# Kernel tuning notes

Measured on AMD Instinct MI355X. Metric: run time of the kernel, lower is better.

## Reference

```python
import jax, jax.numpy as jnp
import numpy as np

N_NODES = 50000
N_EDGES = 800000
D_FEAT = 64


def setup_inputs() -> dict:
    key = jax.random.key(0)
    k_x, k_e, k_w = jax.random.split(key, 3)
    x = jax.random.normal(k_x, (N_NODES, D_FEAT), dtype=jnp.float32)
    edge_index = jax.random.randint(k_e, (2, N_EDGES), 0, N_NODES, dtype=jnp.int64)
    # message MLP params (phi_Theta): single linear + ReLU
    W = jax.random.normal(k_w, (D_FEAT, D_FEAT), dtype=jnp.float32) / np.sqrt(D_FEAT)
    b = jnp.zeros((D_FEAT,), dtype=jnp.float32)
    return {"x": x, "edge_index": edge_index, "W": W, "b": b}


def reference(x, edge_index, W, b):
    # flow = source_to_target: messages flow from edge_index[0] (j) to edge_index[1] (i)
    src = edge_index[0]  # j: source nodes (gather)
    dst = edge_index[1]  # i: target nodes (scatter index)
    n_nodes = x.shape[0]
    # __collect__: index_select gather of source node features -> x_j [E, D]
    x_j = x[src]
    # message: per-edge MLP  phi(x_j) = relu(x_j W + b)
    msg = jax.nn.relu(jnp.einsum('ed,df->ef', x_j, W) + b)
    # aggregate: scatter-add into target nodes (aggr='add', dim_size = size_i)
    out = jax.ops.segment_sum(msg, dst, num_segments=n_nodes)
    # update: identity
    return out
```

## Files before the change

### kernel.cpp

```cpp
#include <hip/hip_runtime.h>
#include <hip/hip_bf16.h>

#define D 64
#define CAP 32
#define OVF_CAP 16384
#define NSHARD 8

__device__ __forceinline__ float bf2f(unsigned short u) {
    return __uint_as_float((unsigned int)u << 16);
}
__device__ __forceinline__ unsigned short f2bf(float f) {
    unsigned int u = __float_as_uint(f);
    unsigned int r = (u + 0x7fffu + ((u >> 16) & 1u)) >> 16;
    return (unsigned short)r;
}

__global__ __launch_bounds__(256) void node_mlp_kernel(
    const float* __restrict__ x, const float* __restrict__ W,
    const float* __restrict__ b, unsigned short* __restrict__ m0,
    unsigned short* __restrict__ m1, int* __restrict__ cnt,
    int* __restrict__ ovf_cnt, int n_nodes) {
    for (int i = blockIdx.x * blockDim.x + threadIdx.x; i < n_nodes;
         i += gridDim.x * blockDim.x) cnt[i] = 0;
    if (blockIdx.x == 0 && threadIdx.x == 0) *ovf_cnt = 0;

    const int lane = threadIdx.x & 63;
    const int l31 = lane & 31;
    unsigned short* mp = (lane < 32) ? m0 : m1;
    float w[D];
    #pragma unroll
    for (int k = 0; k < D; ++k) w[k] = W[k * D + lane];
    const float bias = b[lane];

    const int wave = (blockIdx.x * blockDim.x + threadIdx.x) >> 6;
    const int nwaves = (gridDim.x * blockDim.x) >> 6;

    for (int row = wave; row < n_nodes; row += nwaves) {
        const float4* xr = (const float4*)(x + (size_t)row * D);
        float acc = bias;
        #pragma unroll
        for (int kk = 0; kk < D / 4; ++kk) {
            float4 xv = xr[kk];
            acc = fmaf(xv.x, w[4 * kk + 0], acc);
            acc = fmaf(xv.y, w[4 * kk + 1], acc);
            acc = fmaf(xv.z, w[4 * kk + 2], acc);
            acc = fmaf(xv.w, w[4 * kk + 3], acc);
        }
        mp[(size_t)row * 32 + l31] = f2bf(fmaxf(acc, 0.0f));
    }
}

__global__ __launch_bounds__(256) void append_kernel(
    const int* __restrict__ src, const int* __restrict__ dst,
    int* __restrict__ cnt, unsigned short* __restrict__ slots,
    int* __restrict__ ovf_cnt, unsigned int* __restrict__ ovf,
    int n_edges, int blocks_per_shard) {
    const int shard = blockIdx.x & (NSHARD - 1);
    const int p = blockIdx.x >> 3;
    const int chunk = (n_edges + blocks_per_shard - 1) / blocks_per_shard;
    const int beg = p * chunk;
    const int end = min(beg + chunk, n_edges);

    for (int e = beg + (int)threadIdx.x; e < end; e += 256) {
        int d = dst[e];
        if ((d & (NSHARD - 1)) != shard) continue;
        int s = src[e];
        int pos = atomicAdd(&cnt[d], 1);
        if (pos < CAP) {
            slots[(size_t)d * CAP + pos] = (unsigned short)s;
        } else {
            int op = atomicAdd(ovf_cnt, 1);
            if (op < OVF_CAP)
                ovf[op] = ((unsigned int)d << 16) | (unsigned int)s;
        }
    }
}

__global__ __launch_bounds__(256) void gather_kernel(
    const unsigned short* __restrict__ slots, const int* __restrict__ cnt,
    const unsigned short* __restrict__ m0, const unsigned short* __restrict__ m1,
    const int* __restrict__ ovf_cnt, const unsigned int* __restrict__ ovf,
    float* __restrict__ out, int n_nodes) {
    int node = blockIdx.x * 4 + (threadIdx.x >> 6);
    if (node >= n_nodes) return;
    node = __builtin_amdgcn_readfirstlane(node);

    const int lane = threadIdx.x & 63;
    const int l31 = lane & 31;
    const unsigned short* __restrict__ mplane = (lane < 32) ? m0 : m1;

    const int c = cnt[node];
    const int cc = min(c, CAP);
    const unsigned int* __restrict__ row =
        (const unsigned int*)(slots + (size_t)node * CAP);

    float acc = 0.0f;
    int k = 0;
    for (; k + 8 <= cc; k += 8) {
        unsigned int p0 = row[(k >> 1) + 0];
        unsigned int p1 = row[(k >> 1) + 1];
        unsigned int p2 = row[(k >> 1) + 2];
        unsigned int p3 = row[(k >> 1) + 3];
        unsigned int s0 = p0 & 0xFFFFu, s1 = p0 >> 16;
        unsigned int s2 = p1 & 0xFFFFu, s3 = p1 >> 16;
        unsigned int s4 = p2 & 0xFFFFu, s5 = p2 >> 16;
        unsigned int s6 = p3 & 0xFFFFu, s7 = p3 >> 16;
        float v0 = bf2f(mplane[(size_t)s0 * 32 + l31]);
        float v1 = bf2f(mplane[(size_t)s1 * 32 + l31]);
        float v2 = bf2f(mplane[(size_t)s2 * 32 + l31]);
        float v3 = bf2f(mplane[(size_t)s3 * 32 + l31]);
        float v4 = bf2f(mplane[(size_t)s4 * 32 + l31]);
        float v5 = bf2f(mplane[(size_t)s5 * 32 + l31]);
        float v6 = bf2f(mplane[(size_t)s6 * 32 + l31]);
        float v7 = bf2f(mplane[(size_t)s7 * 32 + l31]);
        acc += ((v0 + v1) + (v2 + v3)) + ((v4 + v5) + (v6 + v7));
    }
    for (; k < cc; ++k) {
        unsigned int p = row[k >> 1];
        unsigned int s = (k & 1) ? (p >> 16) : (p & 0xFFFFu);
        acc += bf2f(mplane[(size_t)s * 32 + l31]);
    }
    if (c > CAP) {
        int oc = min(*ovf_cnt, OVF_CAP);
        for (int i = 0; i < oc; ++i) {
            unsigned int e = ovf[i];
            if ((int)(e >> 16) == node)
                acc += bf2f(mplane[(size_t)(e & 0xFFFFu) * 32 + l31]);
        }
    }
    out[(size_t)node * D + lane] = acc;
}

__global__ __launch_bounds__(256) void edge_scatter_kernel(
    const int* __restrict__ src, const int* __restrict__ dst,
    const unsigned short* __restrict__ m0, const unsigned short* __restrict__ m1,
    float* __restrict__ out, int n_edges) {
    long long t = (long long)blockIdx.x * blockDim.x + threadIdx.x;
    int e = (int)(t >> 4);
    if (e >= n_edges) return;
    int c = (int)(t & 15) << 2;
    int s = src[e];
    int d = dst[e];
    const unsigned short* mp = (c < 32) ? m0 : m1;
    const ushort4 v = *(const ushort4*)(mp + (size_t)s * 32 + (c & 31));
    float* o = out + (size_t)d * D + c;
    atomicAdd(o + 0, bf2f(v.x));
    atomicAdd(o + 1, bf2f(v.y));
    atomicAdd(o + 2, bf2f(v.z));
    atomicAdd(o + 3, bf2f(v.w));
}

static inline size_t align_up(size_t v, size_t a) { return (v + a - 1) & ~(a - 1); }

extern "C" void kernel_launch(void* const* d_in, const int* in_sizes, int n_in,
                              void* d_out, int out_size, void* d_ws, size_t ws_size,
                              hipStream_t stream) {
    const float* x = (const float*)d_in[0];
    const int* edge_index = (const int*)d_in[1];
    const float* W = (const float*)d_in[2];
    const float* b = (const float*)d_in[3];
    float* out = (float*)d_out;

    const int n_nodes = in_sizes[0] / D;
    const int n_edges = in_sizes[1] / 2;
    const int* src = edge_index;
    const int* dst = edge_index + n_edges;

    size_t off = 0;
    unsigned short* m0 = (unsigned short*)((char*)d_ws + off);
    off = align_up(off + (size_t)n_nodes * 32 * sizeof(unsigned short), 256);
    unsigned short* m1 = (unsigned short*)((char*)d_ws + off);
    off = align_up(off + (size_t)n_nodes * 32 * sizeof(unsigned short), 256);
    int* cnt = (int*)((char*)d_ws + off);
    off = align_up(off + (size_t)n_nodes * sizeof(int), 256);
    unsigned short* slots = (unsigned short*)((char*)d_ws + off);
    off = align_up(off + (size_t)n_nodes * CAP * sizeof(unsigned short), 256);
    int* ovf_cnt = (int*)((char*)d_ws + off);
    off = align_up(off + sizeof(int), 256);
    unsigned int* ovf = (unsigned int*)((char*)d_ws + off);
    off = align_up(off + (size_t)OVF_CAP * sizeof(unsigned int), 256);
    const size_t needed = off;

    node_mlp_kernel<<<512, 256, 0, stream>>>(x, W, b, m0, m1, cnt, ovf_cnt, n_nodes);

    if (ws_size >= needed && n_nodes <= 65536) {
        const int blocks_per_shard = 128;
        append_kernel<<<blocks_per_shard * NSHARD, 256, 0, stream>>>(
            src, dst, cnt, slots, ovf_cnt, ovf, n_edges, blocks_per_shard);
        gather_kernel<<<(n_nodes + 3) / 4, 256, 0, stream>>>(
            slots, cnt, m0, m1, ovf_cnt, ovf, out, n_nodes);
    } else {
        hipMemsetAsync(d_out, 0, (size_t)out_size * sizeof(float), stream);
        long long total_threads = (long long)n_edges * 16;
        int scat_blocks = (int)((total_threads + 255) / 256);
        edge_scatter_kernel<<<scat_blocks, 256, 0, stream>>>(src, dst, m0, m1,
                                                             out, n_edges);
    }
}
```

Baseline: 160.9 us.

## Merge split bf16 message planes into one row layout, remap gather nodes per XCD

Stores the per-node bf16 messages as one contiguous 64-wide row instead of two 32-wide half planes, so each gathered neighbour row is a single 128-byte access rather than two separate 64-byte accesses. The gather kernel remaps block-to-node so consecutive blocks (which land on different XCDs) handle interleaved nodes, and unrolls the neighbour loop to 16 loads in flight with a 4-wide remainder. This aims to cut memory transactions and raise memory-level parallelism, at the cost of more registers and a changed node locality pattern across XCD L2 caches.

```diff
diff --git a/kernel.cpp b/kernel.cpp
--- a/kernel.cpp
+++ b/kernel.cpp
@@ -17,16 +17,13 @@
 
 __global__ __launch_bounds__(256) void node_mlp_kernel(
     const float* __restrict__ x, const float* __restrict__ W,
-    const float* __restrict__ b, unsigned short* __restrict__ m0,
-    unsigned short* __restrict__ m1, int* __restrict__ cnt,
-    int* __restrict__ ovf_cnt, int n_nodes) {
+    const float* __restrict__ b, unsigned short* __restrict__ m,
+    int* __restrict__ cnt, int* __restrict__ ovf_cnt, int n_nodes) {
     for (int i = blockIdx.x * blockDim.x + threadIdx.x; i < n_nodes;
          i += gridDim.x * blockDim.x) cnt[i] = 0;
     if (blockIdx.x == 0 && threadIdx.x == 0) *ovf_cnt = 0;
 
     const int lane = threadIdx.x & 63;
-    const int l31 = lane & 31;
-    unsigned short* mp = (lane < 32) ? m0 : m1;
     float w[D];
     #pragma unroll
     for (int k = 0; k < D; ++k) w[k] = W[k * D + lane];
@@ -46,7 +43,7 @@
             acc = fmaf(xv.z, w[4 * kk + 2], acc);
             acc = fmaf(xv.w, w[4 * kk + 3], acc);
         }
-        mp[(size_t)row * 32 + l31] = f2bf(fmaxf(acc, 0.0f));
+        m[(size_t)row * D + lane] = f2bf(fmaxf(acc, 0.0f));
     }
 }
 
@@ -78,16 +75,16 @@
 
 __global__ __launch_bounds__(256) void gather_kernel(
     const unsigned short* __restrict__ slots, const int* __restrict__ cnt,
-    const unsigned short* __restrict__ m0, const unsigned short* __restrict__ m1,
+    const unsigned short* __restrict__ m,
     const int* __restrict__ ovf_cnt, const unsigned int* __restrict__ ovf,
     float* __restrict__ out, int n_nodes) {
-    int node = blockIdx.x * 4 + (threadIdx.x >> 6);
+    const int grp = blockIdx.x >> 3;
+    const int xcd = blockIdx.x & 7;
+    int node = grp * 32 + ((threadIdx.x >> 6) << 3) + xcd;
     if (node >= n_nodes) return;
     node = __builtin_amdgcn_readfirstlane(node);
 
     const int lane = threadIdx.x & 63;
-    const int l31 = lane & 31;
-    const unsigned short* __restrict__ mplane = (lane < 32) ? m0 : m1;
 
     const int c = cnt[node];
     const int cc = min(c, CAP);
@@ -96,36 +93,46 @@
 
     float acc = 0.0f;
     int k = 0;
-    for (; k + 8 <= cc; k += 8) {
+    for (; k + 16 <= cc; k += 16) {
+        unsigned int p[8];
+        #pragma unroll
+        for (int i = 0; i < 8; ++i) p[i] = row[(k >> 1) + i];
+        float v[16];
+        #pragma unroll
+        for (int i = 0; i < 8; ++i) {
+            const unsigned short* ba = m + (size_t)(p[i] & 0xFFFFu) * D;
+            const unsigned short* bb = m + (size_t)(p[i] >> 16) * D;
+            v[2 * i + 0] = bf2f(ba[lane]);
+            v[2 * i + 1] = bf2f(bb[lane]);
+        }
+        float t0 = ((v[0] + v[1]) + (v[2] + v[3])) + ((v[4] + v[5]) + (v[6] + v[7]));
+        float t1 = ((v[8] + v[9]) + (v[10] + v[11])) + ((v[12] + v[13]) + (v[14] + v[15]));
+        acc += t0 + t1;
+    }
+    for (; k + 4 <= cc; k += 4) {
         unsigned int p0 = row[(k >> 1) + 0];
         unsigned int p1 = row[(k >> 1) + 1];
-        unsigned int p2 = row[(k >> 1) + 2];
-        unsigned int p3 = row[(k >> 1) + 3];
-        unsigned int s0 = p0 & 0xFFFFu, s1 = p0 >> 16;
-        unsigned int s2 = p1 & 0xFFFFu, s3 = p1 >> 16;
-        unsigned int s4 = p2 & 0xFFFFu, s5 = p2 >> 16;
-        unsigned int s6 = p3 & 0xFFFFu, s7 = p3 >> 16;
-        float v0 = bf2f(mplane[(size_t)s0 * 32 + l31]);
-        float v1 = bf2f(mplane[(size_t)s1 * 32 + l31]);
-        float v2 = bf2f(mplane[(size_t)s2 * 32 + l31]);
-        float v3 = bf2f(mplane[(size_t)s3 * 32 + l31]);
-        float v4 = bf2f(mplane[(size_t)s4 * 32 + l31]);
-        float v5 = bf2f(mplane[(size_t)s5 * 32 + l31]);
-        float v6 = bf2f(mplane[(size_t)s6 * 32 + l31]);
-        float v7 = bf2f(mplane[(size_t)s7 * 32 + l31]);
-        acc += ((v0 + v1) + (v2 + v3)) + ((v4 + v5) + (v6 + v7));
+        const unsigned short* b0 = m + (size_t)(p0 & 0xFFFFu) * D;
+        const unsigned short* b1 = m + (size_t)(p0 >> 16) * D;
+        const unsigned short* b2 = m + (size_t)(p1 & 0xFFFFu) * D;
+        const unsigned short* b3 = m + (size_t)(p1 >> 16) * D;
+        float v0 = bf2f(b0[lane]);
+        float v1 = bf2f(b1[lane]);
+        float v2 = bf2f(b2[lane]);
+        float v3 = bf2f(b3[lane]);
+        acc += (v0 + v1) + (v2 + v3);
     }
     for (; k < cc; ++k) {
         unsigned int p = row[k >> 1];
         unsigned int s = (k & 1) ? (p >> 16) : (p & 0xFFFFu);
-        acc += bf2f(mplane[(size_t)s * 32 + l31]);
+        acc += bf2f(m[(size_t)s * D + lane]);
     }
     if (c > CAP) {
         int oc = min(*ovf_cnt, OVF_CAP);
         for (int i = 0; i < oc; ++i) {
             unsigned int e = ovf[i];
             if ((int)(e >> 16) == node)
-                acc += bf2f(mplane[(size_t)(e & 0xFFFFu) * 32 + l31]);
+                acc += bf2f(m[(size_t)(e & 0xFFFFu) * D + lane]);
         }
     }
     out[(size_t)node * D + lane] = acc;
@@ -133,16 +140,14 @@
 
 __global__ __launch_bounds__(256) void edge_scatter_kernel(
     const int* __restrict__ src, const int* __restrict__ dst,
-    const unsigned short* __restrict__ m0, const unsigned short* __restrict__ m1,
-    float* __restrict__ out, int n_edges) {
+    const unsigned short* __restrict__ m, float* __restrict__ out, int n_edges) {
     long long t = (long long)blockIdx.x * blockDim.x + threadIdx.x;
     int e = (int)(t >> 4);
     if (e >= n_edges) return;
     int c = (int)(t & 15) << 2;
     int s = src[e];
     int d = dst[e];
-    const unsigned short* mp = (c < 32) ? m0 : m1;
-    const ushort4 v = *(const ushort4*)(mp + (size_t)s * 32 + (c & 31));
+    const ushort4 v = *(const ushort4*)(m + (size_t)s * D + c);
     float* o = out + (size_t)d * D + c;
     atomicAdd(o + 0, bf2f(v.x));
     atomicAdd(o + 1, bf2f(v.y));
@@ -167,10 +172,8 @@
     const int* dst = edge_index + n_edges;
 
     size_t off = 0;
-    unsigned short* m0 = (unsigned short*)((char*)d_ws + off);
-    off = align_up(off + (size_t)n_nodes * 32 * sizeof(unsigned short), 256);
-    unsigned short* m1 = (unsigned short*)((char*)d_ws + off);
-    off = align_up(off + (size_t)n_nodes * 32 * sizeof(unsigned short), 256);
+    unsigned short* m = (unsigned short*)((char*)d_ws + off);
+    off = align_up(off + (size_t)n_nodes * D * sizeof(unsigned short), 256);
     int* cnt = (int*)((char*)d_ws + off);
     off = align_up(off + (size_t)n_nodes * sizeof(int), 256);
     unsigned short* slots = (unsigned short*)((char*)d_ws + off);
@@ -181,19 +184,19 @@
     off = align_up(off + (size_t)OVF_CAP * sizeof(unsigned int), 256);
     const size_t needed = off;
 
-    node_mlp_kernel<<<512, 256, 0, stream>>>(x, W, b, m0, m1, cnt, ovf_cnt, n_nodes);
+    node_mlp_kernel<<<512, 256, 0, stream>>>(x, W, b, m, cnt, ovf_cnt, n_nodes);
 
     if (ws_size >= needed && n_nodes <= 65536) {
         const int blocks_per_shard = 128;
         append_kernel<<<blocks_per_shard * NSHARD, 256, 0, stream>>>(
             src, dst, cnt, slots, ovf_cnt, ovf, n_edges, blocks_per_shard);
-        gather_kernel<<<(n_nodes + 3) / 4, 256, 0, stream>>>(
-            slots, cnt, m0, m1, ovf_cnt, ovf, out, n_nodes);
+        const int ngroups = (n_nodes + 31) / 32;
+        gather_kernel<<<ngroups * 8, 256, 0, stream>>>(
+            slots, cnt, m, ovf_cnt, ovf, out, n_nodes);
     } else {
         hipMemsetAsync(d_out, 0, (size_t)out_size * sizeof(float), stream);
         long long total_threads = (long long)n_edges * 16;
         int scat_blocks = (int)((total_threads + 255) / 256);
-        edge_scatter_kernel<<<scat_blocks, 256, 0, stream>>>(src, dst, m0, m1,
-                                                             out, n_edges);
-    }
-}
+        edge_scatter_kernel<<<scat_blocks, 256, 0, stream>>>(src, dst, m, out, n_edges);
+    }
+}
```

Result: faster. 156.4 us (-2.8%).
